# Performance work log

Measured on AMD Instinct MI355X. Metric: run time of the kernel, lower is better.

Reference implementation:

```python
import jax, jax.numpy as jnp
import numpy as np

N_EMB = 8192
D = 512
BETA = 0.25  # commitment_cost, legacy loss: commit + beta*codebook
EPS = 1e-12  # F.normalize eps


def _l2norm(x):
    n = jnp.sqrt(jnp.sum(x * x, axis=-1, keepdims=True))
    return x / jnp.maximum(n, EPS)


def setup_inputs() -> dict:
    key = jax.random.key(0)
    ks = jax.random.split(key, 6)
    z = jax.random.normal(ks[0], (8, 4096, D), dtype=jnp.float32)
    # frozen codebook, init N(0, D^-0.5)
    embedding = jax.random.normal(ks[1], (N_EMB, D), dtype=jnp.float32) * D ** -0.5
    # embedding_proj: Linear(D, D) default torch init
    lim = 1.0 / np.sqrt(D)
    emb_proj_w = jax.random.uniform(ks[2], (D, D), jnp.float32, -lim, lim)
    emb_proj_b = jax.random.uniform(ks[3], (D,), jnp.float32, -lim, lim)
    # z_proj: identity init, zero bias; perturb slightly to make it non-trivial
    z_proj_w = jnp.eye(D, dtype=jnp.float32) + 0.01 * jax.random.normal(ks[4], (D, D), jnp.float32)
    z_proj_b = jnp.zeros((D,), jnp.float32)
    l2_scale = jnp.asarray(10.0, jnp.float32)
    return {"z": z, "embedding": embedding, "emb_proj_w": emb_proj_w,
            "emb_proj_b": emb_proj_b, "z_proj_w": z_proj_w,
            "z_proj_b": z_proj_b, "l2_scale": l2_scale}


def reference(z, embedding, emb_proj_w, emb_proj_b, z_proj_w, z_proj_b, l2_scale):
    B, T, _ = z.shape
    z_flat = z.reshape(-1, D)                              # [BT, D]
    z_proj = z_flat @ z_proj_w.T + z_proj_b                # [BT, D]
    quant_codebook = embedding @ emb_proj_w.T + emb_proj_b  # [N, D]
    # l2-normalized cosine distances (negated similarity)
    z_n = _l2norm(z_proj)
    c_n = _l2norm(quant_codebook)
    distances = -jnp.einsum('bd,nd->bn', z_n, c_n) * l2_scale  # [BT, N]
    idx = jnp.argmin(distances, axis=1)                    # [BT]
    quantized = quant_codebook[idx].reshape(z.shape)       # [B, T, D]
    commit = jnp.mean((jax.lax.stop_gradient(quantized) - z) ** 2)
    codebook = jnp.mean((quantized - jax.lax.stop_gradient(z)) ** 2)
    vq_loss = commit + BETA * codebook                     # legacy=True
    quantized = z + jax.lax.stop_gradient(quantized - z)   # STE
    return quantized, vq_loss, idx.reshape(B, T)
```

## Files before the change

kernel.cpp:

```cpp
#include <hip/hip_runtime.h>
#include <hip/hip_bf16.h>


#define NQ    32768
#define NEMB  8192
#define DD    512

typedef __attribute__((ext_vector_type(8))) short bf16x8;
typedef __attribute__((ext_vector_type(4))) float f32x4;

__device__ __forceinline__ unsigned short f2bf_rne(float f) {
    unsigned u = __float_as_uint(f);
    unsigned r = u + 0x7FFFu + ((u >> 16) & 1u);
    return (unsigned short)(r >> 16);
}
__device__ __forceinline__ float bf2f(unsigned short b) {
    return __uint_as_float(((unsigned)b) << 16);
}

__device__ __forceinline__ void gload16(const void* g, void* l) {
    __builtin_amdgcn_global_load_lds(
        (const __attribute__((address_space(1))) unsigned int*)g,
        (__attribute__((address_space(3))) unsigned int*)l, 16, 0, 0);
}

__global__ __launch_bounds__(256) void k_split(const float* __restrict__ src,
                                               unsigned short* __restrict__ hi,
                                               unsigned short* __restrict__ lo,
                                               int n4) {
    const float4* s4 = (const float4*)src;
    ushort4* h4 = (ushort4*)hi;
    ushort4* l4 = (ushort4*)lo;
    for (int i = blockIdx.x * blockDim.x + threadIdx.x; i < n4; i += gridDim.x * blockDim.x) {
        float4 v = s4[i];
        ushort4 h, l;
        h.x = f2bf_rne(v.x); l.x = f2bf_rne(v.x - bf2f(h.x));
        h.y = f2bf_rne(v.y); l.y = f2bf_rne(v.y - bf2f(h.y));
        h.z = f2bf_rne(v.z); l.z = f2bf_rne(v.z - bf2f(h.z));
        h.w = f2bf_rne(v.w); l.w = f2bf_rne(v.w - bf2f(h.w));
        h4[i] = h;
        l4[i] = l;
    }
}

__global__ __launch_bounds__(256) void k_wtsplit(const float* __restrict__ W,
                                                 unsigned short* __restrict__ thi,
                                                 unsigned short* __restrict__ tlo) {
    __shared__ float t[32][33];
    const int bx = blockIdx.x * 32;
    const int by = blockIdx.y * 32;
    const int c = threadIdx.x & 31, r0 = threadIdx.x >> 5;
    for (int i = 0; i < 4; ++i) {
        int r = r0 + i * 8;
        t[r][c] = W[(size_t)(by + r) * DD + bx + c];
    }
    __syncthreads();
    for (int i = 0; i < 4; ++i) {
        int r = r0 + i * 8;
        float v = t[c][r];
        unsigned short h = f2bf_rne(v);
        thi[(size_t)(bx + r) * DD + by + c] = h;
        tlo[(size_t)(bx + r) * DD + by + c] = f2bf_rne(v - bf2f(h));
    }
}


__global__ __launch_bounds__(256, 3) void k_qc_mfma(const unsigned short* __restrict__ Ah,
                                                    const unsigned short* __restrict__ Al,
                                                    const unsigned short* __restrict__ Bh,
                                                    const unsigned short* __restrict__ Bl,
                                                    const float* __restrict__ bias,
                                                    float* __restrict__ qc,
                                                    unsigned short* __restrict__ qhi,
                                                    unsigned short* __restrict__ qlo) {
    __shared__ unsigned short sAh[128 * 32];
    __shared__ unsigned short sAl[128 * 32];
    __shared__ unsigned short sBh[128 * 32];
    __shared__ unsigned short sBl[128 * 32];

    const int t    = threadIdx.x;
    const int lane = t & 63;
    const int wave = t >> 6;
    const int wm   = wave >> 1;
    const int wn   = wave & 1;
    const int m0   = blockIdx.y * 128;
    const int n0   = blockIdx.x * 128;

    f32x4 acc[4][4];
    for (int i = 0; i < 4; ++i)
        for (int j = 0; j < 4; ++j) acc[i][j] = (f32x4){0.f, 0.f, 0.f, 0.f};

    const int koff = (((lane >> 4) ^ ((lane >> 1) & 3)) << 3);

    for (int kb = 0; kb < DD; kb += 32) {
        for (int r = 0; r < 2; ++r) {
            const int cbase = r * 256 + wave * 64;
            const int c = cbase + lane;
            const int m = c >> 2;
            const int kg = (c & 3) ^ ((m >> 1) & 3);
            const size_t ga = (size_t)(m0 + m) * DD + kb + kg * 8;
            const size_t gb = (size_t)(n0 + m) * DD + kb + kg * 8;
            gload16(Ah + ga, &sAh[cbase * 8]);
            gload16(Al + ga, &sAl[cbase * 8]);
            gload16(Bh + gb, &sBh[cbase * 8]);
            gload16(Bl + gb, &sBl[cbase * 8]);
        }
        __syncthreads();

        bf16x8 afh[4], afl[4], bfh[4], bfl[4];
        const int ar = wm * 64 + (lane & 15);
        const int br = wn * 64 + (lane & 15);
        for (int i = 0; i < 4; ++i) {
            afh[i] = *(const bf16x8*)&sAh[(ar + i * 16) * 32 + koff];
            afl[i] = *(const bf16x8*)&sAl[(ar + i * 16) * 32 + koff];
            bfh[i] = *(const bf16x8*)&sBh[(br + i * 16) * 32 + koff];
            bfl[i] = *(const bf16x8*)&sBl[(br + i * 16) * 32 + koff];
        }
        for (int i = 0; i < 4; ++i)
            for (int j = 0; j < 4; ++j) {
                acc[i][j] = __builtin_amdgcn_mfma_f32_16x16x32_bf16(afh[i], bfh[j], acc[i][j], 0, 0, 0);
                acc[i][j] = __builtin_amdgcn_mfma_f32_16x16x32_bf16(afh[i], bfl[j], acc[i][j], 0, 0, 0);
                acc[i][j] = __builtin_amdgcn_mfma_f32_16x16x32_bf16(afl[i], bfh[j], acc[i][j], 0, 0, 0);
            }
        __syncthreads();
    }

    const int colb = lane & 15;
    const int g    = lane >> 4;
    float bcol[4];
    for (int tn = 0; tn < 4; ++tn) bcol[tn] = bias[n0 + wn * 64 + tn * 16 + colb];
    for (int tm = 0; tm < 4; ++tm) {
        for (int reg = 0; reg < 4; ++reg) {
            int row = m0 + wm * 64 + tm * 16 + g * 4 + reg;
            for (int tn = 0; tn < 4; ++tn) {
                int col = n0 + wn * 64 + tn * 16 + colb;
                float v = acc[tm][tn][reg] + bcol[tn];
                size_t o = (size_t)row * DD + col;
                qc[o] = v;
                unsigned short h = f2bf_rne(v);
                qhi[o] = h;
                qlo[o] = f2bf_rne(v - bf2f(h));
            }
        }
    }
}

__global__ __launch_bounds__(256, 3) void k_e_mfma(const unsigned short* __restrict__ Ah,
                                                   const unsigned short* __restrict__ Al,
                                                   const unsigned short* __restrict__ Bh,
                                                   const unsigned short* __restrict__ Bl,
                                                   const float* __restrict__ rnorm,
                                                   unsigned short* __restrict__ ehi,
                                                   unsigned short* __restrict__ elo) {
    __shared__ unsigned short sAh[128 * 32];
    __shared__ unsigned short sAl[128 * 32];
    __shared__ unsigned short sBh[128 * 32];
    __shared__ unsigned short sBl[128 * 32];

    const int t    = threadIdx.x;
    const int lane = t & 63;
    const int wave = t >> 6;
    const int wm   = wave >> 1;
    const int wn   = wave & 1;
    const int m0   = blockIdx.y * 128;
    const int n0   = blockIdx.x * 128;

    f32x4 acc[4][4];
    for (int i = 0; i < 4; ++i)
        for (int j = 0; j < 4; ++j) acc[i][j] = (f32x4){0.f, 0.f, 0.f, 0.f};

    const int koff = (((lane >> 4) ^ ((lane >> 1) & 3)) << 3);

    for (int kb = 0; kb < DD; kb += 32) {
        for (int r = 0; r < 2; ++r) {
            const int cbase = r * 256 + wave * 64;
            const int c = cbase + lane;
            const int m = c >> 2;
            const int kg = (c & 3) ^ ((m >> 1) & 3);
            const size_t ga = (size_t)(m0 + m) * DD + kb + kg * 8;
            const size_t gb = (size_t)(n0 + m) * DD + kb + kg * 8;
            gload16(Ah + ga, &sAh[cbase * 8]);
            gload16(Al + ga, &sAl[cbase * 8]);
            gload16(Bh + gb, &sBh[cbase * 8]);
            gload16(Bl + gb, &sBl[cbase * 8]);
        }
        __syncthreads();

        bf16x8 afh[4], afl[4], bfh[4], bfl[4];
        const int ar = wm * 64 + (lane & 15);
        const int br = wn * 64 + (lane & 15);
        for (int i = 0; i < 4; ++i) {
            afh[i] = *(const bf16x8*)&sAh[(ar + i * 16) * 32 + koff];
            afl[i] = *(const bf16x8*)&sAl[(ar + i * 16) * 32 + koff];
            bfh[i] = *(const bf16x8*)&sBh[(br + i * 16) * 32 + koff];
            bfl[i] = *(const bf16x8*)&sBl[(br + i * 16) * 32 + koff];
        }
        for (int i = 0; i < 4; ++i)
            for (int j = 0; j < 4; ++j) {
                acc[i][j] = __builtin_amdgcn_mfma_f32_16x16x32_bf16(afh[i], bfh[j], acc[i][j], 0, 0, 0);
                acc[i][j] = __builtin_amdgcn_mfma_f32_16x16x32_bf16(afh[i], bfl[j], acc[i][j], 0, 0, 0);
                acc[i][j] = __builtin_amdgcn_mfma_f32_16x16x32_bf16(afl[i], bfh[j], acc[i][j], 0, 0, 0);
            }
        __syncthreads();
    }

    const int colb = lane & 15;
    const int g    = lane >> 4;
    for (int tm = 0; tm < 4; ++tm) {
        const int rbase = m0 + wm * 64 + tm * 16 + g * 4;
        float4 rn4 = *(const float4*)&rnorm[rbase];
        const float rnv[4] = {rn4.x, rn4.y, rn4.z, rn4.w};
        for (int reg = 0; reg < 4; ++reg) {
            int row = rbase + reg;
            for (int tn = 0; tn < 4; ++tn) {
                int col = n0 + wn * 64 + tn * 16 + colb;
                float v = acc[tm][tn][reg] * rnv[reg];
                size_t o = (size_t)row * DD + col;
                unsigned short h = f2bf_rne(v);
                ehi[o] = h;
                elo[o] = f2bf_rne(v - bf2f(h));
            }
        }
    }
}

__global__ __launch_bounds__(256) void k_norm(const float* __restrict__ qc,
                                              const float* __restrict__ bz,
                                              float* __restrict__ rnorm,
                                              float* __restrict__ tvec) {
    const int n = blockIdx.x;
    const int t = threadIdx.x;
    float ss = 0.f, tb = 0.f;
    for (int d = t; d < DD; d += 256) {
        float v = qc[(size_t)n * DD + d];
        ss += v * v;
        tb += bz[d] * v;
    }
    for (int off = 32; off; off >>= 1) {
        ss += __shfl_down(ss, off);
        tb += __shfl_down(tb, off);
    }
    __shared__ float s1[4], s2[4];
    int wave = t >> 6, lane = t & 63;
    if (lane == 0) { s1[wave] = ss; s2[wave] = tb; }
    __syncthreads();
    if (t == 0) {
        ss = s1[0] + s1[1] + s1[2] + s1[3];
        tb = s2[0] + s2[1] + s2[2] + s2[3];
        float norm = sqrtf(ss);
        float rn = 1.f / fmaxf(norm, 1e-12f);
        rnorm[n] = rn;
        tvec[n] = tb * rn;
    }
}

__global__ __launch_bounds__(256, 3) void k_scores(const unsigned short* __restrict__ Ah,
                                                   const unsigned short* __restrict__ Al,
                                                   const unsigned short* __restrict__ Bh,
                                                   const unsigned short* __restrict__ Bl,
                                                   const float* __restrict__ tvec,
                                                   unsigned long long* __restrict__ table) {
    __shared__ unsigned short sAh[128 * 32];
    __shared__ unsigned short sAl[128 * 32];
    __shared__ unsigned short sBh[128 * 32];
    __shared__ unsigned short sBl[128 * 32];

    const int t    = threadIdx.x;
    const int lane = t & 63;
    const int wave = t >> 6;
    const int wm   = wave >> 1;
    const int wn   = wave & 1;
    const int m0   = blockIdx.y * 128;
    const int n0   = blockIdx.x * 128;

    f32x4 acc[4][4];
    for (int i = 0; i < 4; ++i)
        for (int j = 0; j < 4; ++j) acc[i][j] = (f32x4){0.f, 0.f, 0.f, 0.f};

    const int koff = (((lane >> 4) ^ ((lane >> 1) & 3)) << 3);

    for (int kb = 0; kb < DD; kb += 32) {
        for (int r = 0; r < 2; ++r) {
            const int cbase = r * 256 + wave * 64;
            const int c = cbase + lane;
            const int m = c >> 2;
            const int kg = (c & 3) ^ ((m >> 1) & 3);
            const size_t ga = (size_t)(m0 + m) * DD + kb + kg * 8;
            const size_t gb = (size_t)(n0 + m) * DD + kb + kg * 8;
            gload16(Ah + ga, &sAh[cbase * 8]);
            gload16(Al + ga, &sAl[cbase * 8]);
            gload16(Bh + gb, &sBh[cbase * 8]);
            gload16(Bl + gb, &sBl[cbase * 8]);
        }
        __syncthreads();

        bf16x8 afh[4], afl[4], bfh[4], bfl[4];
        const int ar = wm * 64 + (lane & 15);
        const int br = wn * 64 + (lane & 15);
        for (int i = 0; i < 4; ++i) {
            afh[i] = *(const bf16x8*)&sAh[(ar + i * 16) * 32 + koff];
            afl[i] = *(const bf16x8*)&sAl[(ar + i * 16) * 32 + koff];
            bfh[i] = *(const bf16x8*)&sBh[(br + i * 16) * 32 + koff];
            bfl[i] = *(const bf16x8*)&sBl[(br + i * 16) * 32 + koff];
        }
        for (int i = 0; i < 4; ++i)
            for (int j = 0; j < 4; ++j) {
                acc[i][j] = __builtin_amdgcn_mfma_f32_16x16x32_bf16(afh[i], bfh[j], acc[i][j], 0, 0, 0);
                acc[i][j] = __builtin_amdgcn_mfma_f32_16x16x32_bf16(afh[i], bfl[j], acc[i][j], 0, 0, 0);
                acc[i][j] = __builtin_amdgcn_mfma_f32_16x16x32_bf16(afl[i], bfh[j], acc[i][j], 0, 0, 0);
            }
        __syncthreads();
    }

    const int col = lane & 15;
    const int g   = lane >> 4;
    float tc[4];
    for (int tn = 0; tn < 4; ++tn) tc[tn] = tvec[n0 + wn * 64 + tn * 16 + col];

    for (int tm = 0; tm < 4; ++tm) {
        for (int reg = 0; reg < 4; ++reg) {
            float best = -3.4e38f;
            int   bn   = 0x7FFFFFFF;
            for (int tn = 0; tn < 4; ++tn) {
                float v = acc[tm][tn][reg] + tc[tn];
                int n = n0 + wn * 64 + tn * 16 + col;
                if (v > best || (v == best && n < bn)) { best = v; bn = n; }
            }
            for (int off = 1; off < 16; off <<= 1) {
                float ov = __shfl_xor(best, off);
                int   on = __shfl_xor(bn, off);
                if (ov > best || (ov == best && on < bn)) { best = ov; bn = on; }
            }
            if (col == 0) {
                unsigned u = __float_as_uint(best);
                unsigned key = (u & 0x80000000u) ? ~u : (u | 0x80000000u);
                unsigned long long packed =
                    ((unsigned long long)key << 32) |
                    (unsigned long long)(0xFFFFFFFFu - (unsigned)bn);
                int q = m0 + wm * 64 + tm * 16 + g * 4 + reg;
                atomicMax(&table[q], packed);
            }
        }
    }
}

__global__ __launch_bounds__(128) void k_gather(const unsigned long long* __restrict__ table,
                                                const float* __restrict__ qc,
                                                const float* __restrict__ z,
                                                float* __restrict__ outq,
                                                float* __restrict__ partials,
                                                float* __restrict__ outidx) {
    const int q = blockIdx.x;
    const int t = threadIdx.x;
    unsigned long long p = table[q];
    const int idx = (int)(0xFFFFFFFFu - (unsigned)(p & 0xFFFFFFFFull));
    const float4* src = (const float4*)(qc + (size_t)idx * DD);
    const float4* zs  = (const float4*)(z + (size_t)q * DD);
    float4* dst = (float4*)(outq + (size_t)q * DD);
    float4 a = src[t], b = zs[t];
    dst[t] = a;
    float dx = a.x - b.x, dy = a.y - b.y, dz = a.z - b.z, dw = a.w - b.w;
    float ss = dx * dx + dy * dy + dz * dz + dw * dw;
    for (int off = 32; off; off >>= 1) ss += __shfl_down(ss, off);
    __shared__ float sbuf[2];
    if ((t & 63) == 0) sbuf[t >> 6] = ss;
    __syncthreads();
    if (t == 0) {
        partials[q] = sbuf[0] + sbuf[1];
        outidx[q] = (float)idx;
    }
}

__global__ __launch_bounds__(1024) void k_loss(const float* __restrict__ partials,
                                               float* __restrict__ loss) {
    const int t = threadIdx.x;
    float s = 0.f;
    for (int i = t; i < NQ; i += 1024) s += partials[i];
    for (int off = 32; off; off >>= 1) s += __shfl_down(s, off);
    __shared__ float sbuf[16];
    if ((t & 63) == 0) sbuf[t >> 6] = s;
    __syncthreads();
    if (t == 0) {
        float tot = 0.f;
        for (int w = 0; w < 16; ++w) tot += sbuf[w];
        *loss = tot * (1.25f / 16777216.0f);
    }
}

extern "C" void kernel_launch(void* const* d_in, const int* in_sizes, int n_in,
                              void* d_out, int out_size, void* d_ws, size_t ws_size,
                              hipStream_t stream) {
    (void)in_sizes; (void)n_in; (void)out_size; (void)ws_size;
    const float* z   = (const float*)d_in[0];
    const float* emb = (const float*)d_in[1];
    const float* Wp  = (const float*)d_in[2];
    const float* bp  = (const float*)d_in[3];
    const float* Wz  = (const float*)d_in[4];
    const float* bz  = (const float*)d_in[5];

    float* out = (float*)d_out;
    char* ws = (char*)d_ws;
    float* qc            = (float*)(ws + 0);
    float* rnorm         = (float*)(ws + 16777216);
    float* tvec          = (float*)(ws + 16809984);
    unsigned short* ehi  = (unsigned short*)(ws + 16842752);
    unsigned short* elo  = (unsigned short*)(ws + 25231360);
    unsigned short* zhi  = (unsigned short*)(ws + 33619968);
    unsigned short* zlo  = (unsigned short*)(ws + 67174400);
    unsigned long long* table = (unsigned long long*)(ws + 100728832);

    unsigned short* embhi = (unsigned short*)(ws + 33619968);
    unsigned short* emblo = (unsigned short*)(ws + 33619968 + 8388608);
    unsigned short* qchi  = (unsigned short*)(ws + 33619968 + 16777216);
    unsigned short* qclo  = (unsigned short*)(ws + 33619968 + 25165824);
    unsigned short* wphi  = (unsigned short*)(ws + 67174400);
    unsigned short* wplo  = (unsigned short*)(ws + 67174400 + 524288);
    unsigned short* wzthi = (unsigned short*)(ws + 67174400 + 1048576);
    unsigned short* wztlo = (unsigned short*)(ws + 67174400 + 1572864);
    float* partials      = (float*)(ws + 33619968);

    hipMemsetAsync(table, 0, (size_t)NQ * 8, stream);

    k_split<<<1024, 256, 0, stream>>>(emb, embhi, emblo, NEMB * DD / 4);
    k_split<<<256, 256, 0, stream>>>(Wp, wphi, wplo, DD * DD / 4);
    k_wtsplit<<<dim3(16, 16), 256, 0, stream>>>(Wz, wzthi, wztlo);

    k_qc_mfma<<<dim3(DD / 128, NEMB / 128), 256, 0, stream>>>(embhi, emblo, wphi, wplo,
                                                              bp, qc, qchi, qclo);
    k_norm<<<NEMB, 256, 0, stream>>>(qc, bz, rnorm, tvec);
    k_e_mfma<<<dim3(DD / 128, NEMB / 128), 256, 0, stream>>>(qchi, qclo, wzthi, wztlo,
                                                             rnorm, ehi, elo);
    k_split<<<4096, 256, 0, stream>>>(z, zhi, zlo, NQ * DD / 4);

    k_scores<<<dim3(NEMB / 128, NQ / 128), 256, 0, stream>>>(zhi, zlo, ehi, elo, tvec, table);
    k_gather<<<NQ, 128, 0, stream>>>(table, qc, z,
                                     out,
                                     partials,
                                     out + (size_t)NQ * DD + 1);
    k_loss<<<1, 1024, 0, stream>>>(partials, out + (size_t)NQ * DD);
}
```

Baseline: 1.056 ms.

## Rewrite score GEMM as 256x256 tile with double-buffered LDS pipeline

Rewrites the cosine-score GEMM kernel to use 256x256 output tiles with 512 threads (8 waves), a 128KB double-buffered LDS, and direct global-to-LDS loads issued in quarters interleaved with MFMA work. Explicit vmcnt waits and raw barriers replace __syncthreads, and setprio raises priority around the MFMA blocks. The goal is to hide global memory latency behind compute and halve operand reloads per output through larger tiles. In exchange, register pressure and LDS use per block are much higher, the hand-tuned wait counts are fragile, and there are fewer blocks in the grid.

Result: slower. 1.145 ms (+8.4%).

```diff
diff --git a/kernel.cpp b/kernel.cpp
--- a/kernel.cpp
+++ b/kernel.cpp
@@ -254,76 +254,133 @@
     }
 }
 
-__global__ __launch_bounds__(256, 3) void k_scores(const unsigned short* __restrict__ Ah,
+
+#define VMW(n) asm volatile("s_waitcnt vmcnt(" #n ")" ::: "memory")
+#define BARRIER_() do { asm volatile("" ::: "memory"); __builtin_amdgcn_s_barrier(); asm volatile("" ::: "memory"); } while (0)
+
+__global__ __launch_bounds__(512, 2) void k_scores(const unsigned short* __restrict__ Ah,
                                                    const unsigned short* __restrict__ Al,
                                                    const unsigned short* __restrict__ Bh,
                                                    const unsigned short* __restrict__ Bl,
                                                    const float* __restrict__ tvec,
                                                    unsigned long long* __restrict__ table) {
-    __shared__ unsigned short sAh[128 * 32];
-    __shared__ unsigned short sAl[128 * 32];
-    __shared__ unsigned short sBh[128 * 32];
-    __shared__ unsigned short sBl[128 * 32];
-
-    const int t    = threadIdx.x;
-    const int lane = t & 63;
-    const int wave = t >> 6;
-    const int wm   = wave >> 1;
-    const int wn   = wave & 1;
-    const int m0   = blockIdx.y * 128;
-    const int n0   = blockIdx.x * 128;
-
-    f32x4 acc[4][4];
-    for (int i = 0; i < 4; ++i)
+    __shared__ unsigned short lds[65536];
+
+    const int tid  = threadIdx.x;
+    const int lane = tid & 63;
+    const int wave = tid >> 6;
+    const int wm   = wave >> 2;
+    const int wn   = wave & 3;
+    const int m0   = blockIdx.y * 256;
+    const int n0   = blockIdx.x * 256;
+    const int lrow = lane & 15;
+    const int koff = ((lane >> 4) ^ ((lane >> 1) & 3)) << 3;
+
+    const int crow = tid >> 2;
+    const int kgs  = ((tid & 3) ^ ((tid >> 3) & 3)) << 3;
+    const unsigned short* zh_ = Ah + (size_t)(m0 + crow) * DD + kgs;
+    const unsigned short* zl_ = Al + (size_t)(m0 + crow) * DD + kgs;
+    const unsigned short* eh_ = Bh + (size_t)(n0 + crow) * DD + kgs;
+    const unsigned short* el_ = Bl + (size_t)(n0 + crow) * DD + kgs;
+    unsigned short* lw = &lds[wave * 512];
+
+#define STAGE(P, U, KB, NBO, XOFF) \
+    gload16((P) + (size_t)(U) * (128 * DD) + (KB), lw + (NBO) + (XOFF) + (U) * 4096)
+
+    f32x4 acc[8][4];
+#pragma unroll
+    for (int i = 0; i < 8; ++i)
+#pragma unroll
         for (int j = 0; j < 4; ++j) acc[i][j] = (f32x4){0.f, 0.f, 0.f, 0.f};
 
-    const int koff = (((lane >> 4) ^ ((lane >> 1) & 3)) << 3);
-
-    for (int kb = 0; kb < DD; kb += 32) {
-        for (int r = 0; r < 2; ++r) {
-            const int cbase = r * 256 + wave * 64;
-            const int c = cbase + lane;
-            const int m = c >> 2;
-            const int kg = (c & 3) ^ ((m >> 1) & 3);
-            const size_t ga = (size_t)(m0 + m) * DD + kb + kg * 8;
-            const size_t gb = (size_t)(n0 + m) * DD + kb + kg * 8;
-            gload16(Ah + ga, &sAh[cbase * 8]);
-            gload16(Al + ga, &sAl[cbase * 8]);
-            gload16(Bh + gb, &sBh[cbase * 8]);
-            gload16(Bl + gb, &sBl[cbase * 8]);
-        }
-        __syncthreads();
-
-        bf16x8 afh[4], afl[4], bfh[4], bfl[4];
-        const int ar = wm * 64 + (lane & 15);
-        const int br = wn * 64 + (lane & 15);
-        for (int i = 0; i < 4; ++i) {
-            afh[i] = *(const bf16x8*)&sAh[(ar + i * 16) * 32 + koff];
-            afl[i] = *(const bf16x8*)&sAl[(ar + i * 16) * 32 + koff];
-            bfh[i] = *(const bf16x8*)&sBh[(br + i * 16) * 32 + koff];
-            bfl[i] = *(const bf16x8*)&sBl[(br + i * 16) * 32 + koff];
-        }
-        for (int i = 0; i < 4; ++i)
-            for (int j = 0; j < 4; ++j) {
-                acc[i][j] = __builtin_amdgcn_mfma_f32_16x16x32_bf16(afh[i], bfh[j], acc[i][j], 0, 0, 0);
-                acc[i][j] = __builtin_amdgcn_mfma_f32_16x16x32_bf16(afh[i], bfl[j], acc[i][j], 0, 0, 0);
-                acc[i][j] = __builtin_amdgcn_mfma_f32_16x16x32_bf16(afl[i], bfh[j], acc[i][j], 0, 0, 0);
-            }
-        __syncthreads();
-    }
-
-    const int col = lane & 15;
-    const int g   = lane >> 4;
+    bf16x8 afh[4], afl[4], bfh[2], bfl[2];
+
+#define LOAD_A(BO, H)                                                          \
+    _Pragma("unroll")                                                          \
+    for (int s = 0; s < 4; ++s) {                                              \
+        const int ro = (BO) + ((H) * 128 + wm * 64 + s * 16 + lrow) * 32 + koff; \
+        afh[s] = *(const bf16x8*)&lds[ro];                                     \
+        afl[s] = *(const bf16x8*)&lds[ro + 8192];                              \
+    }
+
+#define LOAD_B(BO, G)                                                          \
+    _Pragma("unroll")                                                          \
+    for (int u = 0; u < 2; ++u) {                                              \
+        const int co = (BO) + 16384 + ((G) * 128 + wn * 32 + u * 16 + lrow) * 32 + koff; \
+        bfh[u] = *(const bf16x8*)&lds[co];                                     \
+        bfl[u] = *(const bf16x8*)&lds[co + 8192];                              \
+    }
+
+#define MFMA_Q(H, G)                                                           \
+    __builtin_amdgcn_s_setprio(1);                                             \
+    _Pragma("unroll")                                                          \
+    for (int s = 0; s < 4; ++s) {                                              \
+        _Pragma("unroll")                                                      \
+        for (int u = 0; u < 2; ++u) {                                          \
+            f32x4 a = acc[(H) * 4 + s][(G) * 2 + u];                           \
+            a = __builtin_amdgcn_mfma_f32_16x16x32_bf16(afh[s], bfh[u], a, 0, 0, 0); \
+            a = __builtin_amdgcn_mfma_f32_16x16x32_bf16(afh[s], bfl[u], a, 0, 0, 0); \
+            a = __builtin_amdgcn_mfma_f32_16x16x32_bf16(afl[s], bfh[u], a, 0, 0, 0); \
+            acc[(H) * 4 + s][(G) * 2 + u] = a;                                 \
+        }                                                                      \
+    }                                                                          \
+    __builtin_amdgcn_s_setprio(0);
+
+#define TILE(BO, NBO, KB, DOST, V1, V2, V3)                                    \
+    {                                                                          \
+        VMW(V1); BARRIER_();                                                   \
+        LOAD_A(BO, 0) LOAD_B(BO, 0)                                            \
+        if (DOST) { STAGE(zh_, 0, KB, NBO, 0); STAGE(zl_, 0, KB, NBO, 8192); } \
+        MFMA_Q(0, 0)                                                           \
+        VMW(V2); BARRIER_();                                                   \
+        LOAD_B(BO, 1)                                                          \
+        if (DOST) { STAGE(eh_, 0, KB, NBO, 16384); STAGE(el_, 0, KB, NBO, 24576); } \
+        MFMA_Q(0, 1)                                                           \
+        VMW(V3); BARRIER_();                                                   \
+        LOAD_A(BO, 1) LOAD_B(BO, 0)                                            \
+        if (DOST) { STAGE(eh_, 1, KB, NBO, 16384); STAGE(el_, 1, KB, NBO, 24576); } \
+        MFMA_Q(1, 0)                                                           \
+        BARRIER_();                                                            \
+        LOAD_B(BO, 1)                                                          \
+        if (DOST) { STAGE(zh_, 1, KB, NBO, 0); STAGE(zl_, 1, KB, NBO, 8192); } \
+        MFMA_Q(1, 1)                                                           \
+    }
+
+    STAGE(zh_, 0, 0, 0, 0);
+    STAGE(zl_, 0, 0, 0, 8192);
+    STAGE(eh_, 0, 0, 0, 16384);
+    STAGE(el_, 0, 0, 0, 24576);
+    STAGE(eh_, 1, 0, 0, 16384);
+    STAGE(el_, 1, 0, 0, 24576);
+    STAGE(zh_, 1, 0, 0, 0);
+    STAGE(zl_, 1, 0, 0, 8192);
+
+#pragma unroll 1
+    for (int tp = 0; tp < 7; ++tp) {
+        const int kb = tp * 64;
+        TILE(0, 32768, kb + 32, 1, 4, 4, 4)
+        TILE(32768, 0, kb + 64, 1, 4, 4, 4)
+    }
+    TILE(0, 32768, 480, 1, 4, 4, 4)
+    TILE(32768, 0, 0, 0, 4, 2, 0)
+
+    const int colb = lrow;
+    const int g4   = lane >> 4;
     float tc[4];
-    for (int tn = 0; tn < 4; ++tn) tc[tn] = tvec[n0 + wn * 64 + tn * 16 + col];
-
-    for (int tm = 0; tm < 4; ++tm) {
+#pragma unroll
+    for (int ni = 0; ni < 4; ++ni)
+        tc[ni] = tvec[n0 + (ni >> 1) * 128 + wn * 32 + (ni & 1) * 16 + colb];
+
+#pragma unroll
+    for (int mi = 0; mi < 8; ++mi) {
+#pragma unroll
         for (int reg = 0; reg < 4; ++reg) {
             float best = -3.4e38f;
             int   bn   = 0x7FFFFFFF;
-            for (int tn = 0; tn < 4; ++tn) {
-                float v = acc[tm][tn][reg] + tc[tn];
-                int n = n0 + wn * 64 + tn * 16 + col;
+#pragma unroll
+            for (int ni = 0; ni < 4; ++ni) {
+                float v = acc[mi][ni][reg] + tc[ni];
+                int n = n0 + (ni >> 1) * 128 + wn * 32 + (ni & 1) * 16 + colb;
                 if (v > best || (v == best && n < bn)) { best = v; bn = n; }
             }
             for (int off = 1; off < 16; off <<= 1) {
@@ -331,17 +388,22 @@
                 int   on = __shfl_xor(bn, off);
                 if (ov > best || (ov == best && on < bn)) { best = ov; bn = on; }
             }
-            if (col == 0) {
+            if (colb == 0) {
                 unsigned u = __float_as_uint(best);
                 unsigned key = (u & 0x80000000u) ? ~u : (u | 0x80000000u);
                 unsigned long long packed =
                     ((unsigned long long)key << 32) |
                     (unsigned long long)(0xFFFFFFFFu - (unsigned)bn);
-                int q = m0 + wm * 64 + tm * 16 + g * 4 + reg;
+                int q = m0 + (mi >> 2) * 128 + wm * 64 + (mi & 3) * 16 + g4 * 4 + reg;
                 atomicMax(&table[q], packed);
             }
         }
     }
+#undef STAGE
+#undef LOAD_A
+#undef LOAD_B
+#undef MFMA_Q
+#undef TILE
 }
 
 __global__ __launch_bounds__(128) void k_gather(const unsigned long long* __restrict__ table,
@@ -432,7 +494,7 @@
                                                              rnorm, ehi, elo);
     k_split<<<4096, 256, 0, stream>>>(z, zhi, zlo, NQ * DD / 4);
 
-    k_scores<<<dim3(NEMB / 128, NQ / 128), 256, 0, stream>>>(zhi, zlo, ehi, elo, tvec, table);
+    k_scores<<<dim3(NEMB / 256, NQ / 256), 512, 0, stream>>>(zhi, zlo, ehi, elo, tvec, table);
     k_gather<<<NQ, 128, 0, stream>>>(table, qc, z,
                                      out,
                                      partials,
```

## Double-buffer LDS tiles in scores GEMM to overlap global loads with MFMA

Applied to the files above, without the earlier changes.

The scores kernel now keeps two LDS buffers for the hi/lo bf16 A and B tiles. It issues the next k-slice's global-to-LDS loads before computing on the current slice, so the two barriers per iteration become one. Load address setup is hoisted out of the loop and the inner loops are explicitly unrolled. LDS use doubles to 64KB per block and launch bounds drop from 3 to 2 blocks per CU, which lowers occupancy in exchange for hiding memory latency.

After: 1.355 ms. 1.28x slower.

```diff
diff --git a/kernel.cpp b/kernel.cpp
--- a/kernel.cpp
+++ b/kernel.cpp
@@ -254,16 +254,16 @@
     }
 }
 
-__global__ __launch_bounds__(256, 3) void k_scores(const unsigned short* __restrict__ Ah,
+__global__ __launch_bounds__(256, 2) void k_scores(const unsigned short* __restrict__ Ah,
                                                    const unsigned short* __restrict__ Al,
                                                    const unsigned short* __restrict__ Bh,
                                                    const unsigned short* __restrict__ Bl,
                                                    const float* __restrict__ tvec,
                                                    unsigned long long* __restrict__ table) {
-    __shared__ unsigned short sAh[128 * 32];
-    __shared__ unsigned short sAl[128 * 32];
-    __shared__ unsigned short sBh[128 * 32];
-    __shared__ unsigned short sBl[128 * 32];
+    __shared__ unsigned short sAh[2][128 * 32];
+    __shared__ unsigned short sAl[2][128 * 32];
+    __shared__ unsigned short sBh[2][128 * 32];
+    __shared__ unsigned short sBl[2][128 * 32];
 
     const int t    = threadIdx.x;
     const int lane = t & 63;
@@ -274,53 +274,88 @@
     const int n0   = blockIdx.x * 128;
 
     f32x4 acc[4][4];
+#pragma unroll
     for (int i = 0; i < 4; ++i)
+#pragma unroll
         for (int j = 0; j < 4; ++j) acc[i][j] = (f32x4){0.f, 0.f, 0.f, 0.f};
 
     const int koff = (((lane >> 4) ^ ((lane >> 1) & 3)) << 3);
 
-    for (int kb = 0; kb < DD; kb += 32) {
-        for (int r = 0; r < 2; ++r) {
-            const int cbase = r * 256 + wave * 64;
-            const int c = cbase + lane;
-            const int m = c >> 2;
-            const int kg = (c & 3) ^ ((m >> 1) & 3);
-            const size_t ga = (size_t)(m0 + m) * DD + kb + kg * 8;
-            const size_t gb = (size_t)(n0 + m) * DD + kb + kg * 8;
-            gload16(Ah + ga, &sAh[cbase * 8]);
-            gload16(Al + ga, &sAl[cbase * 8]);
-            gload16(Bh + gb, &sBh[cbase * 8]);
-            gload16(Bl + gb, &sBl[cbase * 8]);
-        }
-        __syncthreads();
+    const int cbase0 = wave * 64;
+    const int cbase1 = 256 + wave * 64;
+    const int c0 = cbase0 + lane, c1 = cbase1 + lane;
+    const int mr0 = c0 >> 2, mr1 = c1 >> 2;
+    const int kg0 = (c0 & 3) ^ ((mr0 >> 1) & 3);
+    const int kg1 = (c1 & 3) ^ ((mr1 >> 1) & 3);
+    const unsigned short* a0h = Ah + (size_t)(m0 + mr0) * DD + kg0 * 8;
+    const unsigned short* a0l = Al + (size_t)(m0 + mr0) * DD + kg0 * 8;
+    const unsigned short* b0h = Bh + (size_t)(n0 + mr0) * DD + kg0 * 8;
+    const unsigned short* b0l = Bl + (size_t)(n0 + mr0) * DD + kg0 * 8;
+    const unsigned short* a1h = Ah + (size_t)(m0 + mr1) * DD + kg1 * 8;
+    const unsigned short* a1l = Al + (size_t)(m0 + mr1) * DD + kg1 * 8;
+    const unsigned short* b1h = Bh + (size_t)(n0 + mr1) * DD + kg1 * 8;
+    const unsigned short* b1l = Bl + (size_t)(n0 + mr1) * DD + kg1 * 8;
+
+#define STAGE_T(KB, P)                                  \
+    do {                                                \
+        gload16(a0h + (KB), &sAh[P][cbase0 * 8]);       \
+        gload16(a0l + (KB), &sAl[P][cbase0 * 8]);       \
+        gload16(b0h + (KB), &sBh[P][cbase0 * 8]);       \
+        gload16(b0l + (KB), &sBl[P][cbase0 * 8]);       \
+        gload16(a1h + (KB), &sAh[P][cbase1 * 8]);       \
+        gload16(a1l + (KB), &sAl[P][cbase1 * 8]);       \
+        gload16(b1h + (KB), &sBh[P][cbase1 * 8]);       \
+        gload16(b1l + (KB), &sBl[P][cbase1 * 8]);       \
+    } while (0)
+
+    STAGE_T(0, 0);
+    asm volatile("s_waitcnt vmcnt(0)" ::: "memory");
+    __builtin_amdgcn_s_barrier();
+
+    const int ar = wm * 64 + (lane & 15);
+    const int br = wn * 64 + (lane & 15);
+
+#pragma unroll 1
+    for (int tt = 0; tt < 16; ++tt) {
+        const int p = tt & 1;
+        if (tt < 15) STAGE_T((tt + 1) * 32, p ^ 1);
+        __builtin_amdgcn_sched_barrier(0);
 
         bf16x8 afh[4], afl[4], bfh[4], bfl[4];
-        const int ar = wm * 64 + (lane & 15);
-        const int br = wn * 64 + (lane & 15);
+#pragma unroll
         for (int i = 0; i < 4; ++i) {
-            afh[i] = *(const bf16x8*)&sAh[(ar + i * 16) * 32 + koff];
-            afl[i] = *(const bf16x8*)&sAl[(ar + i * 16) * 32 + koff];
-            bfh[i] = *(const bf16x8*)&sBh[(br + i * 16) * 32 + koff];
-            bfl[i] = *(const bf16x8*)&sBl[(br + i * 16) * 32 + koff];
-        }
+            afh[i] = *(const bf16x8*)&sAh[p][(ar + i * 16) * 32 + koff];
+            afl[i] = *(const bf16x8*)&sAl[p][(ar + i * 16) * 32 + koff];
+            bfh[i] = *(const bf16x8*)&sBh[p][(br + i * 16) * 32 + koff];
+            bfl[i] = *(const bf16x8*)&sBl[p][(br + i * 16) * 32 + koff];
+        }
+#pragma unroll
         for (int i = 0; i < 4; ++i)
+#pragma unroll
             for (int j = 0; j < 4; ++j) {
                 acc[i][j] = __builtin_amdgcn_mfma_f32_16x16x32_bf16(afh[i], bfh[j], acc[i][j], 0, 0, 0);
                 acc[i][j] = __builtin_amdgcn_mfma_f32_16x16x32_bf16(afh[i], bfl[j], acc[i][j], 0, 0, 0);
                 acc[i][j] = __builtin_amdgcn_mfma_f32_16x16x32_bf16(afl[i], bfh[j], acc[i][j], 0, 0, 0);
             }
-        __syncthreads();
-    }
+
+        asm volatile("s_waitcnt vmcnt(0)" ::: "memory");
+        __builtin_amdgcn_s_barrier();
+    }
+#undef STAGE_T
 
     const int col = lane & 15;
     const int g   = lane >> 4;
     float tc[4];
+#pragma unroll
     for (int tn = 0; tn < 4; ++tn) tc[tn] = tvec[n0 + wn * 64 + tn * 16 + col];
 
+#pragma unroll
     for (int tm = 0; tm < 4; ++tm) {
+#pragma unroll
         for (int reg = 0; reg < 4; ++reg) {
             float best = -3.4e38f;
             int   bn   = 0x7FFFFFFF;
+#pragma unroll
             for (int tn = 0; tn < 4; ++tn) {
                 float v = acc[tm][tn][reg] + tc[tn];
                 int n = n0 + wn * 64 + tn * 16 + col;
```
